# Kernel tuning notes

Measured on AMD Instinct MI355X. Metric: run time of the kernel, lower is better.

Reference implementation:

```python
import jax, jax.numpy as jnp
import numpy as np

B_, T_, L_, M_, H_, F_ = 16, 2048, 128, 256, 512, 1024
EPS = 1e-5


def _init_reservoir(h, rng):
    # orthogonal matrix scaled inside the unit disk for a stable linear recurrence
    q, _ = np.linalg.qr(rng.standard_normal((h, h)).astype(np.float32))
    return jnp.asarray(0.95 * q, dtype=jnp.float32)


def setup_inputs() -> dict:
    key = jax.random.key(0)
    ks = jax.random.split(key, 8)
    rng = np.random.default_rng(0)
    s = lambda fan_in: 1.0 / np.sqrt(fan_in)
    return {
        "x": jax.random.normal(ks[0], (B_, T_, L_), dtype=jnp.float32),
        "We": jax.random.uniform(ks[1], (L_, M_), jnp.float32, -s(L_), s(L_)),
        "be": jnp.zeros((M_,), jnp.float32),
        "Wb": jax.random.uniform(ks[2], (M_, H_), jnp.float32, -s(M_), s(M_)),
        "A": _init_reservoir(H_, rng),
        "Wr": jax.random.uniform(ks[3], (L_, H_), jnp.float32, -s(L_), s(L_)),
        "br": jnp.zeros((H_,), jnp.float32),
        "ln_g": jnp.ones((H_,), jnp.float32),
        "ln_b": jnp.zeros((H_,), jnp.float32),
        "W1": jax.random.uniform(ks[4], (H_, F_), jnp.float32, -s(H_), s(H_)),
        "b1": jnp.zeros((F_,), jnp.float32),
        "W2": jax.random.uniform(ks[5], (F_, H_), jnp.float32, -s(F_), s(F_)),
        "b2": jnp.zeros((H_,), jnp.float32),
    }


def reference(x, We, be, Wb, A, Wr, br, ln_g, ln_b, W1, b1, W2, b2):
    # encoder + B projection, batched over all timesteps: [B,T,H]
    Bu = (x @ We + be) @ Wb

    # sequential linear recurrence h_t = h_{t-1} @ A + Bu_t, h_0 = Bu_0
    def step(h, bu_t):
        h = h @ A + bu_t
        return h, h

    h0 = jnp.zeros((x.shape[0], A.shape[0]), x.dtype)
    _, Hs = jax.lax.scan(step, h0, jnp.swapaxes(Bu, 0, 1))  # [T,B,H]
    H_seq = jnp.swapaxes(Hs, 0, 1)  # [B,T,H]

    # residual + layer norm
    z = H_seq + (x @ Wr + br)
    mu = jnp.mean(z, axis=-1, keepdims=True)
    var = jnp.mean(jnp.square(z - mu), axis=-1, keepdims=True)
    zn = (z - mu) * jax.lax.rsqrt(var + EPS) * ln_g + ln_b

    # MLP on last timestep
    h_last = zn[:, -1, :]
    out = jax.nn.relu(h_last @ W1 + b1) @ W2 + b2
    return out
```

## Files before the change

kernel.cpp:

```cpp
#include <hip/hip_runtime.h>

#define B_  16
#define T_  2048
#define L_  128
#define M_  256
#define H_  512
#define F_  1024
#define EPS 1e-5f

#define LDA_S 36
#define LDB_S 68
#define SMSZ (64 * LDA_S + 64 * LDB_S)

__device__ __forceinline__ float4 load_a4(const float* __restrict__ A,
                                          const float* __restrict__ Alast,
                                          int M, int lda, int amode,
                                          int gr, int gk) {
    float4 av = make_float4(0.f, 0.f, 0.f, 0.f);
    if (gr < M) {
        const float* p;
        if (amode == 1)
            p = A + (long)((gr & 15) * T_ + (T_ - 1 - (gr >> 4))) * L_ + gk;
        else if (amode == 2)
            p = A + (long)(((gr >> 4) << 5) + 16 + (gr & 15)) * lda + gk;
        else if (amode == 3 && gr == M - 1)
            p = Alast + gk;
        else
            p = A + (long)gr * lda + gk;
        av = *(const float4*)p;
    }
    return av;
}

__device__ __forceinline__ void gemm_tile(
    float* sm,
    const float* __restrict__ A, const float* __restrict__ Alast,
    const float* __restrict__ Bm, const float* __restrict__ bias,
    const float* __restrict__ Add, float* __restrict__ C,
    int M, int K, int lda, int ldb, int ldc,
    int flags, int amode, int bx, int by)
{
    constexpr int BM = 32, BN = 64, BK = 64, TM = 2, TN = 4;
    float* As = sm;
    float* Bs = sm + BK * LDA_S;
    const int tid = threadIdx.x;
    const int tx = tid & 15;
    const int ty = tid >> 4;
    const int row0 = by * BM, col0 = bx * BN;

    float4 pa[2], pb[4];
#pragma unroll
    for (int t = 0; t < 2; ++t) {
        int f = tid + t * 256;
        pa[t] = load_a4(A, Alast, M, lda, amode, row0 + (f >> 4), (f & 15) * 4);
    }
#pragma unroll
    for (int t = 0; t < 4; ++t) {
        int f = tid + t * 256;
        pb[t] = *(const float4*)(Bm + (long)(f >> 4) * ldb + col0 + (f & 15) * 4);
    }

    float acc[TM][TN] = {};

    for (int k0 = 0; k0 < K; k0 += BK) {
        __syncthreads();
#pragma unroll
        for (int t = 0; t < 2; ++t) {
            int f = tid + t * 256;
            int arow = f >> 4, kk = (f & 15) * 4;
            As[(kk + 0) * LDA_S + arow] = pa[t].x;
            As[(kk + 1) * LDA_S + arow] = pa[t].y;
            As[(kk + 2) * LDA_S + arow] = pa[t].z;
            As[(kk + 3) * LDA_S + arow] = pa[t].w;
        }
#pragma unroll
        for (int t = 0; t < 4; ++t) {
            int f = tid + t * 256;
            *(float4*)&Bs[(f >> 4) * LDB_S + (f & 15) * 4] = pb[t];
        }
        __syncthreads();
        int kn = k0 + BK;
        if (kn < K) {
#pragma unroll
            for (int t = 0; t < 2; ++t) {
                int f = tid + t * 256;
                pa[t] = load_a4(A, Alast, M, lda, amode, row0 + (f >> 4), kn + (f & 15) * 4);
            }
#pragma unroll
            for (int t = 0; t < 4; ++t) {
                int f = tid + t * 256;
                pb[t] = *(const float4*)(Bm + (long)(kn + (f >> 4)) * ldb + col0 + (f & 15) * 4);
            }
        }
#pragma unroll
        for (int kk = 0; kk < BK; ++kk) {
            float ra[TM], rb[TN];
#pragma unroll
            for (int i = 0; i < TM; ++i) ra[i] = As[kk * LDA_S + ty * TM + i];
#pragma unroll
            for (int j = 0; j < TN; ++j) rb[j] = Bs[kk * LDB_S + tx * TN + j];
#pragma unroll
            for (int i = 0; i < TM; ++i)
#pragma unroll
                for (int j = 0; j < TN; ++j)
                    acc[i][j] = fmaf(ra[i], rb[j], acc[i][j]);
        }
    }

#pragma unroll
    for (int i = 0; i < TM; ++i) {
        int r = row0 + ty * TM + i;
        if (r >= M) continue;
#pragma unroll
        for (int j = 0; j < TN; ++j) {
            int c = col0 + tx * TN + j;
            float v = acc[i][j];
            if (flags & 1) v += bias[c];
            if (amode == 2) v += Add[(long)(((r >> 4) << 5) + (r & 15)) * ldc + c];
            C[(long)r * ldc + c] = v;
        }
    }
}

__global__ __launch_bounds__(256) void dual(
    const float* A, const float* Alast, const float* Bm, const float* bias,
    const float* Add, float* C, int M, int K, int lda, int ldb, int ldc,
    int flags, int amode, int nbxA, int nA,
    const float* SqL, const float* SqR, float* SqOut)
{
    __shared__ float sm[SMSZ];
    int j = blockIdx.x;
    if (j < nA)
        gemm_tile(sm, A, Alast, Bm, bias, Add, C, M, K, lda, ldb, ldc,
                  flags, amode, j % nbxA, j / nbxA);
    else {
        int s = j - nA;
        gemm_tile(sm, SqL, nullptr, SqR, nullptr, nullptr, SqOut,
                  H_, H_, H_, H_, H_, 0, 0, s % 8, s / 8);
    }
}

#define TLDA 20
#define TLDB 68
#define TSM (64 * TLDA + 64 * TLDB)

template <int MODE>
__device__ __forceinline__ float4 tail_a4(const float* __restrict__ Asrc,
                                          const float* __restrict__ x,
                                          int b, int gk) {
    if (MODE == 0) {
        int seg = gk >> 9;
        if (seg < 3)
            return *(const float4*)(Asrc + (long)((seg + 1) * 16 + b) * H_ + (gk & 511));
        return *(const float4*)(x + ((long)b * T_ + (T_ - 1)) * L_ + (gk - 1536));
    } else if (MODE == 1) {
        return *(const float4*)(Asrc + (long)b * H_ + gk);
    } else {
        return *(const float4*)(Asrc + (long)b * F_ + gk);
    }
}

template <int MODE>
__device__ __forceinline__ float4 tail_b4(const float* __restrict__ P32,
                                          const float* __restrict__ P64,
                                          const float* __restrict__ P96,
                                          const float* __restrict__ WrB,
                                          int kr, int c) {
    if (MODE == 0) {
        const float* p;
        if (kr < 512)       p = P32 + (long)kr * H_;
        else if (kr < 1024) p = P64 + (long)(kr - 512) * H_;
        else if (kr < 1536) p = P96 + (long)(kr - 1024) * H_;
        else                p = WrB + (long)(kr - 1536) * H_;
        return *(const float4*)(p + c);
    } else if (MODE == 1) {
        return *(const float4*)(WrB + (long)kr * F_ + c);
    } else {
        return *(const float4*)(WrB + (long)kr * H_ + c);
    }
}

template <int MODE>
__global__ __launch_bounds__(256) void tailgemm(
    const float* __restrict__ Asrc, const float* __restrict__ x,
    const float* __restrict__ P32, const float* __restrict__ P64,
    const float* __restrict__ P96, const float* __restrict__ WrB,
    float* __restrict__ parts, int nbx, int kLen)
{
    constexpr int LDC = (MODE == 1) ? F_ : H_;
    __shared__ float sm[TSM];
    float* As = sm;
    float* Bs = sm + 64 * TLDA;
    const int tid = threadIdx.x;
    const int tx = tid & 15, ty = tid >> 4;
    const int kc = blockIdx.x / nbx;
    const int col0 = (blockIdx.x % nbx) * 64;
    const int kOff = kc * kLen;

    float4 pa, pb[4];
    {
        int gk = kOff + (tid & 15) * 4;
        pa = tail_a4<MODE>(Asrc, x, tid >> 4, gk);
#pragma unroll
        for (int t = 0; t < 4; ++t) {
            int f = tid + t * 256;
            pb[t] = tail_b4<MODE>(P32, P64, P96, WrB, kOff + (f >> 4), col0 + (f & 15) * 4);
        }
    }

    float acc[4] = {};
    for (int k0 = kOff; k0 < kOff + kLen; k0 += 64) {
        __syncthreads();
        {
            int arow = tid >> 4, kk = (tid & 15) * 4;
            As[(kk + 0) * TLDA + arow] = pa.x;
            As[(kk + 1) * TLDA + arow] = pa.y;
            As[(kk + 2) * TLDA + arow] = pa.z;
            As[(kk + 3) * TLDA + arow] = pa.w;
        }
#pragma unroll
        for (int t = 0; t < 4; ++t) {
            int f = tid + t * 256;
            *(float4*)&Bs[(f >> 4) * TLDB + (f & 15) * 4] = pb[t];
        }
        __syncthreads();
        int kn = k0 + 64;
        if (kn < kOff + kLen) {
            pa = tail_a4<MODE>(Asrc, x, tid >> 4, kn + (tid & 15) * 4);
#pragma unroll
            for (int t = 0; t < 4; ++t) {
                int f = tid + t * 256;
                pb[t] = tail_b4<MODE>(P32, P64, P96, WrB, kn + (f >> 4), col0 + (f & 15) * 4);
            }
        }
#pragma unroll
        for (int kk = 0; kk < 64; ++kk) {
            float ra = As[kk * TLDA + ty];
            float4 rb = *(float4*)&Bs[kk * TLDB + tx * 4];
            acc[0] = fmaf(ra, rb.x, acc[0]);
            acc[1] = fmaf(ra, rb.y, acc[1]);
            acc[2] = fmaf(ra, rb.z, acc[2]);
            acc[3] = fmaf(ra, rb.w, acc[3]);
        }
    }

    float* dst = parts + (long)kc * 16 * LDC + (long)ty * LDC + col0 + tx * 4;
    *(float4*)dst = make_float4(acc[0], acc[1], acc[2], acc[3]);
}

__global__ __launch_bounds__(256) void zlnred(
    const float* __restrict__ V1, const float* __restrict__ zparts,
    const float* __restrict__ br, const float* __restrict__ lng,
    const float* __restrict__ lnb, float* __restrict__ zn)
{
    __shared__ float red1[4], red2[4];
    const int b = blockIdx.x, tid = threadIdx.x;
    float z[2];
#pragma unroll
    for (int jj = 0; jj < 2; ++jj) {
        int c = tid + jj * 256;
        float s = V1[(long)b * H_ + c] + br[c];
#pragma unroll
        for (int kc = 0; kc < 13; ++kc)
            s += zparts[(long)kc * 16 * H_ + (long)b * H_ + c];
        z[jj] = s;
    }
    float s1 = z[0] + z[1];
    float s2 = z[0] * z[0] + z[1] * z[1];
#pragma unroll
    for (int off = 32; off > 0; off >>= 1) {
        s1 += __shfl_down(s1, off, 64);
        s2 += __shfl_down(s2, off, 64);
    }
    int wid = tid >> 6, lane = tid & 63;
    if (lane == 0) { red1[wid] = s1; red2[wid] = s2; }
    __syncthreads();
    float S1 = red1[0] + red1[1] + red1[2] + red1[3];
    float S2 = red2[0] + red2[1] + red2[2] + red2[3];
    float mu  = S1 * (1.0f / H_);
    float var = S2 * (1.0f / H_) - mu * mu;
    float rs  = rsqrtf(var + EPS);
#pragma unroll
    for (int jj = 0; jj < 2; ++jj) {
        int c = tid + jj * 256;
        zn[(long)b * H_ + c] = (z[jj] - mu) * rs * lng[c] + lnb[c];
    }
}

__global__ __launch_bounds__(256) void hred(
    const float* __restrict__ h1p, const float* __restrict__ b1,
    float* __restrict__ hid)
{
    int b = blockIdx.x >> 2;
    int c = (blockIdx.x & 3) * 256 + threadIdx.x;
    float s = b1[c];
#pragma unroll
    for (int kc = 0; kc < 4; ++kc)
        s += h1p[(long)kc * 16 * F_ + (long)b * F_ + c];
    hid[(long)b * F_ + c] = fmaxf(s, 0.f);
}

__global__ __launch_bounds__(256) void ored(
    const float* __restrict__ op, const float* __restrict__ b2,
    float* __restrict__ out)
{
    int b = blockIdx.x >> 1;
    int c = (blockIdx.x & 1) * 256 + threadIdx.x;
    float s = b2[c];
#pragma unroll
    for (int kc = 0; kc < 8; ++kc)
        s += op[(long)kc * 16 * H_ + (long)b * H_ + c];
    out[(long)b * H_ + c] = s;
}

extern "C" void kernel_launch(void* const* d_in, const int* in_sizes, int n_in,
                              void* d_out, int out_size, void* d_ws, size_t ws_size,
                              hipStream_t stream) {
    const float* x    = (const float*)d_in[0];
    const float* We   = (const float*)d_in[1];
    const float* be   = (const float*)d_in[2];
    const float* Wb   = (const float*)d_in[3];
    const float* Amat = (const float*)d_in[4];
    const float* Wr   = (const float*)d_in[5];
    const float* br   = (const float*)d_in[6];
    const float* lng  = (const float*)d_in[7];
    const float* lnb  = (const float*)d_in[8];
    const float* W1   = (const float*)d_in[9];
    const float* b1   = (const float*)d_in[10];
    const float* W2   = (const float*)d_in[11];
    const float* b2   = (const float*)d_in[12];
    float* out = (float*)d_out;

    float* ws  = (float*)d_ws;
    float* Wc  = ws;
    float* V0  = Wc + 129 * H_;
    float* V1  = V0 + 2048 * H_;
    float* P2  = V1 + 1024 * H_;
    float* P4  = P2 + H_ * H_;
    float* P8  = P4 + H_ * H_;
    float* P16 = P8 + H_ * H_;
    float* P32 = P16 + H_ * H_;
    float* P64 = P32 + H_ * H_;
    float* P96 = P64 + H_ * H_;
    float* zn  = P96 + H_ * H_;
    float* hid = zn + B_ * H_;
    float* zp  = hid + B_ * F_;
    float* h1p = zp + 13 * B_ * H_;
    float* op  = h1p + 4 * B_ * F_;

    dual<<<168, 256, 0, stream>>>(We, be, Wb, nullptr, nullptr, Wc,
                                  129, M_, M_, H_, H_, 0, 3, 8, 40,
                                  Amat, Amat, P2);
    dual<<<640, 256, 0, stream>>>(x, nullptr, Wc, Wc + 128 * H_, nullptr, V0,
                                  2048, L_, L_, H_, H_, 1, 1, 8, 512,
                                  P2, P2, P4);
    dual<<<384, 256, 0, stream>>>(V0, nullptr, Amat, nullptr, V0, V1,
                                  1024, H_, H_, H_, H_, 0, 2, 8, 256,
                                  P4, P4, P8);
    dual<<<256, 256, 0, stream>>>(V1, nullptr, P2, nullptr, V1, V0,
                                  512, H_, H_, H_, H_, 0, 2, 8, 128,
                                  P8, P8, P16);
    dual<<<192, 256, 0, stream>>>(V0, nullptr, P4, nullptr, V0, V1,
                                  256, H_, H_, H_, H_, 0, 2, 8, 64,
                                  P16, P16, P32);
    dual<<<160, 256, 0, stream>>>(V1, nullptr, P8, nullptr, V1, V0,
                                  128, H_, H_, H_, H_, 0, 2, 8, 32,
                                  P32, P32, P64);
    dual<<<144, 256, 0, stream>>>(V0, nullptr, P16, nullptr, V0, V1,
                                  64, H_, H_, H_, H_, 0, 2, 8, 16,
                                  P32, P64, P96);
    tailgemm<0><<<104, 256, 0, stream>>>(V1, x, P32, P64, P96, Wr, zp, 8, 128);
    zlnred<<<16, 256, 0, stream>>>(V1, zp, br, lng, lnb, zn);
    tailgemm<1><<<64, 256, 0, stream>>>(zn, nullptr, nullptr, nullptr, nullptr,
                                        W1, h1p, 16, 128);
    hred<<<64, 256, 0, stream>>>(h1p, b1, hid);
    tailgemm<2><<<64, 256, 0, stream>>>(hid, nullptr, nullptr, nullptr, nullptr,
                                        W2, op, 8, 128);
    ored<<<32, 256, 0, stream>>>(op, b2, out);
}
```

Before: 284.8 us.

## Restructure recurrence into packed multi-job stages with geometric-sum matrices

Replaces the dual-GEMM doubling scheme with a new decomposition. Packed multi-job stage kernels compute powers of A alongside cumulative sums (I+A, then T-chain products) and a stacked Bu basis, and partial results are folded into the tail GEMMs. The GEMM tile grows to 64x64 with 4x4 register micro-tiles, and the hred kernel is fused into the last tail GEMM's A-load. The intent is fewer, wider launches and less serial work, at the cost of more intermediate matrices, split-K partials and new numerical orderings.

```diff
diff --git a/kernel.cpp b/kernel.cpp
--- a/kernel.cpp
+++ b/kernel.cpp
@@ -3,255 +3,275 @@
 #define B_  16
 #define T_  2048
 #define L_  128
-#define M_  256
 #define H_  512
 #define F_  1024
 #define EPS 1e-5f
 
-#define LDA_S 36
-#define LDB_S 68
-#define SMSZ (64 * LDA_S + 64 * LDB_S)
-
-__device__ __forceinline__ float4 load_a4(const float* __restrict__ A,
-                                          const float* __restrict__ Alast,
-                                          int M, int lda, int amode,
-                                          int gr, int gk) {
-    float4 av = make_float4(0.f, 0.f, 0.f, 0.f);
-    if (gr < M) {
-        const float* p;
-        if (amode == 1)
-            p = A + (long)((gr & 15) * T_ + (T_ - 1 - (gr >> 4))) * L_ + gk;
-        else if (amode == 2)
-            p = A + (long)(((gr >> 4) << 5) + 16 + (gr & 15)) * lda + gk;
-        else if (amode == 3 && gr == M - 1)
-            p = Alast + gk;
-        else
-            p = A + (long)gr * lda + gk;
-        av = *(const float4*)p;
-    }
-    return av;
-}
-
-__device__ __forceinline__ void gemm_tile(
-    float* sm,
-    const float* __restrict__ A, const float* __restrict__ Alast,
-    const float* __restrict__ Bm, const float* __restrict__ bias,
-    const float* __restrict__ Add, float* __restrict__ C,
-    int M, int K, int lda, int ldb, int ldc,
-    int flags, int amode, int bx, int by)
-{
-    constexpr int BM = 32, BN = 64, BK = 64, TM = 2, TN = 4;
+#define GP   68
+#define GSM  (64 * GP * 2)
+
+struct Job {
+    const float* A; const float* Aaux; const float* B;
+    const float* Add; float* C; float* C2;
+    int M, lda, kLen, nbx, nrt, amode, emode;
+};
+
+__device__ __forceinline__ float4 jload(const Job& jb, int gr, int gk) {
+    if (jb.amode == 1) {
+        if (gr < 128)  return *(const float4*)(jb.A + (long)gr * jb.lda + gk);
+        if (gr == 128) return *(const float4*)(jb.Aaux + gk);
+        return make_float4(0.f, 0.f, 0.f, 0.f);
+    } else if (jb.amode == 2) {
+        int j = gr >> 4, b = gr & 15;
+        int i = gk >> 7, inner = gk & 127;
+        int t = T_ - 1 - (16 * j + i);
+        return *(const float4*)(jb.A + ((long)b * T_ + t) * L_ + inner);
+    } else {
+        if (gr >= jb.M) return make_float4(0.f, 0.f, 0.f, 0.f);
+        return *(const float4*)(jb.A + (long)gr * jb.lda + gk);
+    }
+}
+
+__device__ __forceinline__ void g64run(float* sm, const Job& jb, int rel) {
     float* As = sm;
-    float* Bs = sm + BK * LDA_S;
-    const int tid = threadIdx.x;
-    const int tx = tid & 15;
-    const int ty = tid >> 4;
-    const int row0 = by * BM, col0 = bx * BN;
-
-    float4 pa[2], pb[4];
-#pragma unroll
-    for (int t = 0; t < 2; ++t) {
-        int f = tid + t * 256;
-        pa[t] = load_a4(A, Alast, M, lda, amode, row0 + (f >> 4), (f & 15) * 4);
-    }
+    float* Bs = sm + 64 * GP;
+    const int tid = threadIdx.x, tx = tid & 15, ty = tid >> 4;
+    const int bx = rel % jb.nbx;
+    const int r  = rel / jb.nbx;
+    const int by = r % jb.nrt;
+    const int kc = r / jb.nrt;
+    const int row0 = by * 64, col0 = bx * 64, kOff = kc * jb.kLen;
+
+    float4 pa[4], pb[4];
 #pragma unroll
     for (int t = 0; t < 4; ++t) {
         int f = tid + t * 256;
-        pb[t] = *(const float4*)(Bm + (long)(f >> 4) * ldb + col0 + (f & 15) * 4);
-    }
-
-    float acc[TM][TN] = {};
-
-    for (int k0 = 0; k0 < K; k0 += BK) {
+        pa[t] = jload(jb, row0 + (f >> 4), kOff + (f & 15) * 4);
+        pb[t] = *(const float4*)(jb.B + (long)(kOff + (f >> 4)) * H_ + col0 + (f & 15) * 4);
+    }
+    float acc[4][4] = {};
+    for (int k0 = 0; k0 < jb.kLen; k0 += 64) {
         __syncthreads();
-#pragma unroll
-        for (int t = 0; t < 2; ++t) {
-            int f = tid + t * 256;
-            int arow = f >> 4, kk = (f & 15) * 4;
-            As[(kk + 0) * LDA_S + arow] = pa[t].x;
-            As[(kk + 1) * LDA_S + arow] = pa[t].y;
-            As[(kk + 2) * LDA_S + arow] = pa[t].z;
-            As[(kk + 3) * LDA_S + arow] = pa[t].w;
-        }
 #pragma unroll
         for (int t = 0; t < 4; ++t) {
             int f = tid + t * 256;
-            *(float4*)&Bs[(f >> 4) * LDB_S + (f & 15) * 4] = pb[t];
+            int ar = f >> 4, ak = (f & 15) * 4;
+            As[(ak + 0) * GP + ar] = pa[t].x;
+            As[(ak + 1) * GP + ar] = pa[t].y;
+            As[(ak + 2) * GP + ar] = pa[t].z;
+            As[(ak + 3) * GP + ar] = pa[t].w;
+            *(float4*)&Bs[(f >> 4) * GP + (f & 15) * 4] = pb[t];
         }
         __syncthreads();
-        int kn = k0 + BK;
-        if (kn < K) {
-#pragma unroll
-            for (int t = 0; t < 2; ++t) {
-                int f = tid + t * 256;
-                pa[t] = load_a4(A, Alast, M, lda, amode, row0 + (f >> 4), kn + (f & 15) * 4);
-            }
+        int kn = k0 + 64;
+        if (kn < jb.kLen) {
 #pragma unroll
             for (int t = 0; t < 4; ++t) {
                 int f = tid + t * 256;
-                pb[t] = *(const float4*)(Bm + (long)(kn + (f >> 4)) * ldb + col0 + (f & 15) * 4);
+                pa[t] = jload(jb, row0 + (f >> 4), kOff + kn + (f & 15) * 4);
+                pb[t] = *(const float4*)(jb.B + (long)(kOff + kn + (f >> 4)) * H_ +
+                                         col0 + (f & 15) * 4);
             }
         }
 #pragma unroll
-        for (int kk = 0; kk < BK; ++kk) {
-            float ra[TM], rb[TN];
-#pragma unroll
-            for (int i = 0; i < TM; ++i) ra[i] = As[kk * LDA_S + ty * TM + i];
-#pragma unroll
-            for (int j = 0; j < TN; ++j) rb[j] = Bs[kk * LDB_S + tx * TN + j];
-#pragma unroll
-            for (int i = 0; i < TM; ++i)
-#pragma unroll
-                for (int j = 0; j < TN; ++j)
-                    acc[i][j] = fmaf(ra[i], rb[j], acc[i][j]);
-        }
-    }
-
-#pragma unroll
-    for (int i = 0; i < TM; ++i) {
-        int r = row0 + ty * TM + i;
-        if (r >= M) continue;
-#pragma unroll
-        for (int j = 0; j < TN; ++j) {
-            int c = col0 + tx * TN + j;
-            float v = acc[i][j];
-            if (flags & 1) v += bias[c];
-            if (amode == 2) v += Add[(long)(((r >> 4) << 5) + (r & 15)) * ldc + c];
-            C[(long)r * ldc + c] = v;
-        }
-    }
-}
-
-__global__ __launch_bounds__(256) void dual(
-    const float* A, const float* Alast, const float* Bm, const float* bias,
-    const float* Add, float* C, int M, int K, int lda, int ldb, int ldc,
-    int flags, int amode, int nbxA, int nA,
-    const float* SqL, const float* SqR, float* SqOut)
-{
-    __shared__ float sm[SMSZ];
-    int j = blockIdx.x;
-    if (j < nA)
-        gemm_tile(sm, A, Alast, Bm, bias, Add, C, M, K, lda, ldb, ldc,
-                  flags, amode, j % nbxA, j / nbxA);
-    else {
-        int s = j - nA;
-        gemm_tile(sm, SqL, nullptr, SqR, nullptr, nullptr, SqOut,
-                  H_, H_, H_, H_, H_, 0, 0, s % 8, s / 8);
-    }
-}
-
-#define TLDA 20
-#define TLDB 68
-#define TSM (64 * TLDA + 64 * TLDB)
+        for (int kk = 0; kk < 64; ++kk) {
+            float4 ra = *(float4*)&As[kk * GP + ty * 4];
+            float4 rb = *(float4*)&Bs[kk * GP + tx * 4];
+            acc[0][0] = fmaf(ra.x, rb.x, acc[0][0]);
+            acc[0][1] = fmaf(ra.x, rb.y, acc[0][1]);
+            acc[0][2] = fmaf(ra.x, rb.z, acc[0][2]);
+            acc[0][3] = fmaf(ra.x, rb.w, acc[0][3]);
+            acc[1][0] = fmaf(ra.y, rb.x, acc[1][0]);
+            acc[1][1] = fmaf(ra.y, rb.y, acc[1][1]);
+            acc[1][2] = fmaf(ra.y, rb.z, acc[1][2]);
+            acc[1][3] = fmaf(ra.y, rb.w, acc[1][3]);
+            acc[2][0] = fmaf(ra.z, rb.x, acc[2][0]);
+            acc[2][1] = fmaf(ra.z, rb.y, acc[2][1]);
+            acc[2][2] = fmaf(ra.z, rb.z, acc[2][2]);
+            acc[2][3] = fmaf(ra.z, rb.w, acc[2][3]);
+            acc[3][0] = fmaf(ra.w, rb.x, acc[3][0]);
+            acc[3][1] = fmaf(ra.w, rb.y, acc[3][1]);
+            acc[3][2] = fmaf(ra.w, rb.z, acc[3][2]);
+            acc[3][3] = fmaf(ra.w, rb.w, acc[3][3]);
+        }
+    }
+    long coff = (long)kc * jb.M * H_;
+#pragma unroll
+    for (int i = 0; i < 4; ++i) {
+        int rr = row0 + ty * 4 + i;
+        if (rr >= jb.M) continue;
+        int c = col0 + tx * 4;
+        float4 v = make_float4(acc[i][0], acc[i][1], acc[i][2], acc[i][3]);
+        if (jb.Add) {
+            float4 ad = *(const float4*)(jb.Add + (long)rr * H_ + c);
+            v.x += ad.x; v.y += ad.y; v.z += ad.z; v.w += ad.w;
+        }
+        if (jb.emode == 1 && rr == 128)
+            *(float4*)(jb.C2 + c) = v;
+        else
+            *(float4*)(jb.C + coff + (long)rr * H_ + c) = v;
+    }
+}
+
+struct Pack { Job j[4]; int n0, n1, n2, n3; };
+
+__global__ __launch_bounds__(256) void gstage(Pack p) {
+    __shared__ float sm[GSM];
+    int b = blockIdx.x, rel;
+    const Job* jb;
+    if (b < p.n0) { jb = &p.j[0]; rel = b; }
+    else if (b < p.n0 + p.n1) { jb = &p.j[1]; rel = b - p.n0; }
+    else if (b < p.n0 + p.n1 + p.n2) { jb = &p.j[2]; rel = b - p.n0 - p.n1; }
+    else { jb = &p.j[3]; rel = b - p.n0 - p.n1 - p.n2; }
+    if (jb->amode == 9) {
+        for (int idx = rel * 256 + threadIdx.x; idx < H_ * H_; idx += 8 * 256) {
+            int row = idx >> 9, col = idx & 511;
+            jb->C[idx] = jb->A[idx] + (row == col ? 1.f : 0.f);
+        }
+        return;
+    }
+    g64run(sm, *jb, rel);
+}
+
+struct TP {
+    const float* G; const float* Hp; const float* C1; const float* C2p;
+    const float* C3; const float* C4; const float* T7; const float* bc;
+    const float* x; const float* Wr; const float* zn; const float* W1;
+    const float* h1p; const float* b1; const float* W2;
+    float* outp;
+    int nbx, nrg, kLen;
+};
 
 template <int MODE>
-__device__ __forceinline__ float4 tail_a4(const float* __restrict__ Asrc,
-                                          const float* __restrict__ x,
-                                          int b, int gk) {
+__device__ __forceinline__ float4 ta4(const TP& tp, int rg, int b, int gk) {
     if (MODE == 0) {
-        int seg = gk >> 9;
-        if (seg < 3)
-            return *(const float4*)(Asrc + (long)((seg + 1) * 16 + b) * H_ + (gk & 511));
-        return *(const float4*)(x + ((long)b * T_ + (T_ - 1)) * L_ + (gk - 1536));
+        int u = gk >> 9, inner = gk & 511;
+        int r = (4 * rg + u + 1) * 16 + b;
+        float4 s = make_float4(0.f, 0.f, 0.f, 0.f);
+#pragma unroll
+        for (int q = 0; q < 4; ++q) {
+            float4 g = *(const float4*)(tp.G + (long)q * 128 * H_ + (long)r * H_ + inner);
+            s.x += g.x; s.y += g.y; s.z += g.z; s.w += g.w;
+        }
+        return s;
     } else if (MODE == 1) {
-        return *(const float4*)(Asrc + (long)b * H_ + gk);
+        if (gk < 512) {
+            float4 s = make_float4(0.f, 0.f, 0.f, 0.f);
+#pragma unroll
+            for (int q = 0; q < 3; ++q) {
+                float4 h = *(const float4*)(tp.Hp + (long)q * 32 * H_ + (long)(16 + b) * H_ + gk);
+                s.x += h.x; s.y += h.y; s.z += h.z; s.w += h.w;
+            }
+#pragma unroll
+            for (int q = 0; q < 4; ++q) {
+                float4 g = *(const float4*)(tp.G + (long)q * 128 * H_ + (long)(64 + b) * H_ + gk);
+                s.x += g.x; s.y += g.y; s.z += g.z; s.w += g.w;
+            }
+            return s;
+        } else if (gk < 1024) {
+            return *(const float4*)(tp.bc + gk - 512);
+        } else {
+            return *(const float4*)(tp.x + ((long)b * T_ + T_ - 1) * L_ + gk - 1024);
+        }
+    } else if (MODE == 2) {
+        return *(const float4*)(tp.zn + (long)b * H_ + gk);
     } else {
-        return *(const float4*)(Asrc + (long)b * F_ + gk);
+        float4 s = *(const float4*)(tp.b1 + gk);
+#pragma unroll
+        for (int q = 0; q < 4; ++q) {
+            float4 h = *(const float4*)(tp.h1p + (long)q * 16 * F_ + (long)b * F_ + gk);
+            s.x += h.x; s.y += h.y; s.z += h.z; s.w += h.w;
+        }
+        return make_float4(fmaxf(s.x, 0.f), fmaxf(s.y, 0.f),
+                           fmaxf(s.z, 0.f), fmaxf(s.w, 0.f));
     }
 }
 
 template <int MODE>
-__device__ __forceinline__ float4 tail_b4(const float* __restrict__ P32,
-                                          const float* __restrict__ P64,
-                                          const float* __restrict__ P96,
-                                          const float* __restrict__ WrB,
-                                          int kr, int c) {
+__device__ __forceinline__ float4 tb4(const TP& tp, int gk, int c) {
     if (MODE == 0) {
-        const float* p;
-        if (kr < 512)       p = P32 + (long)kr * H_;
-        else if (kr < 1024) p = P64 + (long)(kr - 512) * H_;
-        else if (kr < 1536) p = P96 + (long)(kr - 1024) * H_;
-        else                p = WrB + (long)(kr - 1536) * H_;
-        return *(const float4*)(p + c);
+        int u = gk >> 9, inner = gk & 511;
+        const float* P = (u == 0) ? tp.C1 : (u == 1) ? tp.C2p : tp.C3;
+        return *(const float4*)(P + (long)inner * H_ + c);
     } else if (MODE == 1) {
-        return *(const float4*)(WrB + (long)kr * F_ + c);
+        if (gk < 512)  return *(const float4*)(tp.C4 + (long)gk * H_ + c);
+        if (gk < 1024) return *(const float4*)(tp.T7 + (long)(gk - 512) * H_ + c);
+        return *(const float4*)(tp.Wr + (long)(gk - 1024) * H_ + c);
+    } else if (MODE == 2) {
+        return *(const float4*)(tp.W1 + (long)gk * F_ + c);
     } else {
-        return *(const float4*)(WrB + (long)kr * H_ + c);
-    }
-}
-
-template <int MODE>
-__global__ __launch_bounds__(256) void tailgemm(
-    const float* __restrict__ Asrc, const float* __restrict__ x,
-    const float* __restrict__ P32, const float* __restrict__ P64,
-    const float* __restrict__ P96, const float* __restrict__ WrB,
-    float* __restrict__ parts, int nbx, int kLen)
-{
-    constexpr int LDC = (MODE == 1) ? F_ : H_;
-    __shared__ float sm[TSM];
+        return *(const float4*)(tp.W2 + (long)gk * H_ + c);
+    }
+}
+
+template <int MODE, bool GJOB>
+__global__ __launch_bounds__(256) void tstage(TP tp, Job gj, int nThin) {
+    __shared__ float sm[GSM];
+    int blk = blockIdx.x;
+    if (GJOB && blk >= nThin) { g64run(sm, gj, blk - nThin); return; }
     float* As = sm;
-    float* Bs = sm + 64 * TLDA;
-    const int tid = threadIdx.x;
-    const int tx = tid & 15, ty = tid >> 4;
-    const int kc = blockIdx.x / nbx;
-    const int col0 = (blockIdx.x % nbx) * 64;
-    const int kOff = kc * kLen;
+    float* Bs = sm + 64 * 20;
+    const int tid = threadIdx.x, tx = tid & 15, ty = tid >> 4;
+    const int bx = blk % tp.nbx;
+    const int rr = blk / tp.nbx;
+    const int rg = rr % tp.nrg;
+    const int kc = rr / tp.nrg;
+    const int col0 = bx * 64, kOff = kc * tp.kLen;
+    constexpr int LDC  = (MODE == 2) ? F_ : H_;
+    constexpr int ROWS = (MODE == 0) ? 32 : 16;
 
     float4 pa, pb[4];
-    {
-        int gk = kOff + (tid & 15) * 4;
-        pa = tail_a4<MODE>(Asrc, x, tid >> 4, gk);
+    pa = ta4<MODE>(tp, rg, ty, kOff + tx * 4);
+#pragma unroll
+    for (int t = 0; t < 4; ++t) {
+        int f = tid + t * 256;
+        pb[t] = tb4<MODE>(tp, kOff + (f >> 4), col0 + (f & 15) * 4);
+    }
+    float acc[4] = {};
+    for (int k0 = 0; k0 < tp.kLen; k0 += 64) {
+        __syncthreads();
+        {
+            int kk = tx * 4;
+            As[(kk + 0) * 20 + ty] = pa.x;
+            As[(kk + 1) * 20 + ty] = pa.y;
+            As[(kk + 2) * 20 + ty] = pa.z;
+            As[(kk + 3) * 20 + ty] = pa.w;
+        }
 #pragma unroll
         for (int t = 0; t < 4; ++t) {
             int f = tid + t * 256;
-            pb[t] = tail_b4<MODE>(P32, P64, P96, WrB, kOff + (f >> 4), col0 + (f & 15) * 4);
-        }
-    }
-
-    float acc[4] = {};
-    for (int k0 = kOff; k0 < kOff + kLen; k0 += 64) {
-        __syncthreads();
-        {
-            int arow = tid >> 4, kk = (tid & 15) * 4;
-            As[(kk + 0) * TLDA + arow] = pa.x;
-            As[(kk + 1) * TLDA + arow] = pa.y;
-            As[(kk + 2) * TLDA + arow] = pa.z;
-            As[(kk + 3) * TLDA + arow] = pa.w;
-        }
-#pragma unroll
-        for (int t = 0; t < 4; ++t) {
-            int f = tid + t * 256;
-            *(float4*)&Bs[(f >> 4) * TLDB + (f & 15) * 4] = pb[t];
+            *(float4*)&Bs[(f >> 4) * 68 + (f & 15) * 4] = pb[t];
         }
         __syncthreads();
         int kn = k0 + 64;
-        if (kn < kOff + kLen) {
-            pa = tail_a4<MODE>(Asrc, x, tid >> 4, kn + (tid & 15) * 4);
+        if (kn < tp.kLen) {
+            pa = ta4<MODE>(tp, rg, ty, kOff + kn + tx * 4);
 #pragma unroll
             for (int t = 0; t < 4; ++t) {
                 int f = tid + t * 256;
-                pb[t] = tail_b4<MODE>(P32, P64, P96, WrB, kn + (f >> 4), col0 + (f & 15) * 4);
+                pb[t] = tb4<MODE>(tp, kOff + kn + (f >> 4), col0 + (f & 15) * 4);
             }
         }
 #pragma unroll
         for (int kk = 0; kk < 64; ++kk) {
-            float ra = As[kk * TLDA + ty];
-            float4 rb = *(float4*)&Bs[kk * TLDB + tx * 4];
+            float ra = As[kk * 20 + ty];
+            float4 rb = *(float4*)&Bs[kk * 68 + tx * 4];
             acc[0] = fmaf(ra, rb.x, acc[0]);
             acc[1] = fmaf(ra, rb.y, acc[1]);
             acc[2] = fmaf(ra, rb.z, acc[2]);
             acc[3] = fmaf(ra, rb.w, acc[3]);
         }
     }
-
-    float* dst = parts + (long)kc * 16 * LDC + (long)ty * LDC + col0 + tx * 4;
+    float* dst = tp.outp + (long)kc * ROWS * LDC + (long)(rg * 16 + ty) * LDC +
+                 col0 + tx * 4;
     *(float4*)dst = make_float4(acc[0], acc[1], acc[2], acc[3]);
 }
 
-__global__ __launch_bounds__(256) void zlnred(
-    const float* __restrict__ V1, const float* __restrict__ zparts,
-    const float* __restrict__ br, const float* __restrict__ lng,
-    const float* __restrict__ lnb, float* __restrict__ zn)
+__global__ __launch_bounds__(256) void zln(
+    const float* __restrict__ zp, const float* __restrict__ Hp,
+    const float* __restrict__ G, const float* __restrict__ br,
+    const float* __restrict__ lng, const float* __restrict__ lnb,
+    float* __restrict__ zn)
 {
     __shared__ float red1[4], red2[4];
     const int b = blockIdx.x, tid = threadIdx.x;
@@ -259,10 +279,13 @@
 #pragma unroll
     for (int jj = 0; jj < 2; ++jj) {
         int c = tid + jj * 256;
-        float s = V1[(long)b * H_ + c] + br[c];
-#pragma unroll
-        for (int kc = 0; kc < 13; ++kc)
-            s += zparts[(long)kc * 16 * H_ + (long)b * H_ + c];
+        float s = br[c];
+#pragma unroll
+        for (int q = 0; q < 9; ++q) s += zp[(long)q * 16 * H_ + (long)b * H_ + c];
+#pragma unroll
+        for (int q = 0; q < 3; ++q) s += Hp[(long)q * 32 * H_ + (long)b * H_ + c];
+#pragma unroll
+        for (int q = 0; q < 4; ++q) s += G[(long)q * 128 * H_ + (long)b * H_ + c];
         z[jj] = s;
     }
     float s1 = z[0] + z[1];
@@ -287,19 +310,6 @@
     }
 }
 
-__global__ __launch_bounds__(256) void hred(
-    const float* __restrict__ h1p, const float* __restrict__ b1,
-    float* __restrict__ hid)
-{
-    int b = blockIdx.x >> 2;
-    int c = (blockIdx.x & 3) * 256 + threadIdx.x;
-    float s = b1[c];
-#pragma unroll
-    for (int kc = 0; kc < 4; ++kc)
-        s += h1p[(long)kc * 16 * F_ + (long)b * F_ + c];
-    hid[(long)b * F_ + c] = fmaxf(s, 0.f);
-}
-
 __global__ __launch_bounds__(256) void ored(
     const float* __restrict__ op, const float* __restrict__ b2,
     float* __restrict__ out)
@@ -308,8 +318,7 @@
     int c = (blockIdx.x & 1) * 256 + threadIdx.x;
     float s = b2[c];
 #pragma unroll
-    for (int kc = 0; kc < 8; ++kc)
-        s += op[(long)kc * 16 * H_ + (long)b * H_ + c];
+    for (int q = 0; q < 8; ++q) s += op[(long)q * 16 * H_ + (long)b * H_ + c];
     out[(long)b * H_ + c] = s;
 }
 
@@ -331,50 +340,104 @@
     const float* b2   = (const float*)d_in[12];
     float* out = (float*)d_out;
 
-    float* ws  = (float*)d_ws;
-    float* Wc  = ws;
-    float* V0  = Wc + 129 * H_;
-    float* V1  = V0 + 2048 * H_;
-    float* P2  = V1 + 1024 * H_;
-    float* P4  = P2 + H_ * H_;
-    float* P8  = P4 + H_ * H_;
-    float* P16 = P8 + H_ * H_;
-    float* P32 = P16 + H_ * H_;
-    float* P64 = P32 + H_ * H_;
-    float* P96 = P64 + H_ * H_;
-    float* zn  = P96 + H_ * H_;
-    float* hid = zn + B_ * H_;
-    float* zp  = hid + B_ * F_;
-    float* h1p = zp + 13 * B_ * H_;
-    float* op  = h1p + 4 * B_ * F_;
-
-    dual<<<168, 256, 0, stream>>>(We, be, Wb, nullptr, nullptr, Wc,
-                                  129, M_, M_, H_, H_, 0, 3, 8, 40,
-                                  Amat, Amat, P2);
-    dual<<<640, 256, 0, stream>>>(x, nullptr, Wc, Wc + 128 * H_, nullptr, V0,
-                                  2048, L_, L_, H_, H_, 1, 1, 8, 512,
-                                  P2, P2, P4);
-    dual<<<384, 256, 0, stream>>>(V0, nullptr, Amat, nullptr, V0, V1,
-                                  1024, H_, H_, H_, H_, 0, 2, 8, 256,
-                                  P4, P4, P8);
-    dual<<<256, 256, 0, stream>>>(V1, nullptr, P2, nullptr, V1, V0,
-                                  512, H_, H_, H_, H_, 0, 2, 8, 128,
-                                  P8, P8, P16);
-    dual<<<192, 256, 0, stream>>>(V0, nullptr, P4, nullptr, V0, V1,
-                                  256, H_, H_, H_, H_, 0, 2, 8, 64,
-                                  P16, P16, P32);
-    dual<<<160, 256, 0, stream>>>(V1, nullptr, P8, nullptr, V1, V0,
-                                  128, H_, H_, H_, H_, 0, 2, 8, 32,
-                                  P32, P32, P64);
-    dual<<<144, 256, 0, stream>>>(V0, nullptr, P16, nullptr, V0, V1,
-                                  64, H_, H_, H_, H_, 0, 2, 8, 16,
-                                  P32, P64, P96);
-    tailgemm<0><<<104, 256, 0, stream>>>(V1, x, P32, P64, P96, Wr, zp, 8, 128);
-    zlnred<<<16, 256, 0, stream>>>(V1, zp, br, lng, lnb, zn);
-    tailgemm<1><<<64, 256, 0, stream>>>(zn, nullptr, nullptr, nullptr, nullptr,
-                                        W1, h1p, 16, 128);
-    hred<<<64, 256, 0, stream>>>(h1p, b1, hid);
-    tailgemm<2><<<64, 256, 0, stream>>>(hid, nullptr, nullptr, nullptr, nullptr,
-                                        W2, op, 8, 128);
+    float* ws    = (float*)d_ws;
+    float* stack = ws;
+    float* bc    = stack + 2048 * H_;
+    float* P2    = bc + H_;
+    float* P4    = P2 + H_ * H_;
+    float* P8    = P4 + H_ * H_;
+    float* C1    = P8 + H_ * H_;
+    float* C2p   = C1 + H_ * H_;
+    float* C3    = C2p + H_ * H_;
+    float* C4    = C3 + H_ * H_;
+    float* T1    = C4 + H_ * H_;
+    float* T2    = T1 + H_ * H_;
+    float* T3    = T2 + H_ * H_;
+    float* T4    = T3 + H_ * H_;
+    float* T5    = T4 + H_ * H_;
+    float* T6    = T5 + H_ * H_;
+    float* T7    = T6 + H_ * H_;
+    float* G     = T7 + H_ * H_;
+    float* Hp    = G + 4 * 128 * H_;
+    float* zp    = Hp + 3 * 32 * H_;
+    float* zn    = zp + 9 * B_ * H_;
+    float* h1p   = zn + B_ * H_;
+    float* op    = h1p + 4 * B_ * F_;
+
+    Job dummy = {};
+    dummy.M = 0; dummy.nbx = 1; dummy.nrt = 1; dummy.kLen = 64; dummy.amode = 0;
+
+    {
+        Pack p; p.j[3] = dummy;
+        p.j[0] = {We, be, Wb, nullptr, stack, bc, 129, 256, 256, 8, 3, 1, 1};
+        p.j[1] = {Amat, nullptr, Amat, nullptr, P2, nullptr, 512, 512, 512, 8, 8, 0, 0};
+        p.j[2] = {Amat, nullptr, nullptr, nullptr, T1, nullptr, 512, 512, 64, 1, 1, 9, 0};
+        p.n0 = 24; p.n1 = 64; p.n2 = 8; p.n3 = 0;
+        gstage<<<96, 256, 0, stream>>>(p);
+    }
+    {
+        Pack p; p.j[3] = dummy;
+        p.j[0] = {stack, nullptr, Amat, nullptr, stack + 128 * H_, nullptr, 128, 512, 512, 8, 2, 0, 0};
+        p.j[1] = {P2, nullptr, P2, nullptr, P4, nullptr, 512, 512, 512, 8, 8, 0, 0};
+        p.j[2] = {T1, nullptr, P2, T1, T2, nullptr, 512, 512, 512, 8, 8, 0, 0};
+        p.n0 = 16; p.n1 = 64; p.n2 = 64; p.n3 = 0;
+        gstage<<<144, 256, 0, stream>>>(p);
+    }
+    {
+        Pack p; p.j[3] = dummy;
+        p.j[0] = {stack, nullptr, P2, nullptr, stack + 256 * H_, nullptr, 256, 512, 512, 8, 4, 0, 0};
+        p.j[1] = {P4, nullptr, P4, nullptr, P8, nullptr, 512, 512, 512, 8, 8, 0, 0};
+        p.j[2] = {T2, nullptr, P4, T2, T3, nullptr, 512, 512, 512, 8, 8, 0, 0};
+        p.n0 = 32; p.n1 = 64; p.n2 = 64; p.n3 = 0;
+        gstage<<<160, 256, 0, stream>>>(p);
+    }
+    {
+        Pack p; p.j[3] = dummy;
+        p.j[0] = {stack, nullptr, P4, nullptr, stack + 512 * H_, nullptr, 512, 512, 512, 8, 8, 0, 0};
+        p.j[1] = {P8, nullptr, P8, nullptr, C1, nullptr, 512, 512, 512, 8, 8, 0, 0};
+        p.j[2] = {T3, nullptr, P8, T3, T4, nullptr, 512, 512, 512, 8, 8, 0, 0};
+        p.n0 = 64; p.n1 = 64; p.n2 = 64; p.n3 = 0;
+        gstage<<<192, 256, 0, stream>>>(p);
+    }
+    {
+        Pack p; p.j[3] = dummy;
+        p.j[0] = {stack, nullptr, P8, nullptr, stack + 1024 * H_, nullptr, 1024, 512, 512, 8, 16, 0, 0};
+        p.j[1] = {C1, nullptr, C1, nullptr, C2p, nullptr, 512, 512, 512, 8, 8, 0, 0};
+        p.j[2] = {T4, nullptr, C1, T4, T5, nullptr, 512, 512, 512, 8, 8, 0, 0};
+        p.n0 = 128; p.n1 = 64; p.n2 = 64; p.n3 = 0;
+        gstage<<<256, 256, 0, stream>>>(p);
+    }
+    {
+        Pack p;
+        p.j[0] = {x, nullptr, stack, nullptr, G, nullptr, 128, 0, 512, 8, 2, 2, 0};
+        p.j[1] = {C1, nullptr, C2p, nullptr, C3, nullptr, 512, 512, 512, 8, 8, 0, 0};
+        p.j[2] = {C2p, nullptr, C2p, nullptr, C4, nullptr, 512, 512, 512, 8, 8, 0, 0};
+        p.j[3] = {T5, nullptr, C2p, T5, T6, nullptr, 512, 512, 512, 8, 8, 0, 0};
+        p.n0 = 64; p.n1 = 64; p.n2 = 64; p.n3 = 64;
+        gstage<<<256, 256, 0, stream>>>(p);
+    }
+    TP tp;
+    tp.G = G; tp.Hp = Hp; tp.C1 = C1; tp.C2p = C2p; tp.C3 = C3; tp.C4 = C4;
+    tp.T7 = T7; tp.bc = bc; tp.x = x; tp.Wr = Wr; tp.zn = zn; tp.W1 = W1;
+    tp.h1p = h1p; tp.b1 = b1; tp.W2 = W2;
+
+    {
+        TP t = tp; t.outp = Hp; t.nbx = 8; t.nrg = 2; t.kLen = 512;
+        Job gj = {T6, nullptr, C4, T6, T7, nullptr, 512, 512, 512, 8, 8, 0, 0};
+        tstage<0, true><<<48 + 64, 256, 0, stream>>>(t, gj, 48);
+    }
+    {
+        TP t = tp; t.outp = zp; t.nbx = 8; t.nrg = 1; t.kLen = 128;
+        tstage<1, false><<<72, 256, 0, stream>>>(t, dummy, 1 << 30);
+    }
+    zln<<<16, 256, 0, stream>>>(zp, Hp, G, br, lng, lnb, zn);
+    {
+        TP t = tp; t.outp = h1p; t.nbx = 16; t.nrg = 1; t.kLen = 128;
+        tstage<2, false><<<64, 256, 0, stream>>>(t, dummy, 1 << 30);
+    }
+    {
+        TP t = tp; t.outp = op; t.nbx = 8; t.nrg = 1; t.kLen = 128;
+        tstage<3, false><<<64, 256, 0, stream>>>(t, dummy, 1 << 30);
+    }
     ored<<<32, 256, 0, stream>>>(op, b2, out);
 }
```

After: 428.2 us. +50.3%, slower.
